# Kernel optimization log

Hardware: AMD Instinct MI355X
Metric: run time of the kernel (lower is better)

The kernel has to match this reference:

```python
import jax, jax.numpy as jnp
import numpy as np

COMPRESSION = 2  # max-pool factor along flattened spatial axis for phi and g


def setup_inputs() -> dict:
    key = jax.random.key(0)
    ks = jax.random.split(key, 5)
    B, C, H, W = 4, 64, 96, 96
    Ci = 32  # intermediate_dim = C // 2
    s = 1.0 / np.sqrt(C)
    return {
        "x": jax.random.normal(ks[0], (B, C, H, W), dtype=jnp.float32),
        "w_theta": jax.random.normal(ks[1], (Ci, C), dtype=jnp.float32) * s,
        "b_theta": jnp.zeros((Ci,), dtype=jnp.float32),
        "w_phi": jax.random.normal(ks[2], (Ci, C), dtype=jnp.float32) * s,
        "b_phi": jnp.zeros((Ci,), dtype=jnp.float32),
        "w_g": jax.random.normal(ks[3], (Ci, C), dtype=jnp.float32) * s,
        "b_g": jnp.zeros((Ci,), dtype=jnp.float32),
        "w_out": jax.random.normal(ks[4], (C, Ci), dtype=jnp.float32) * (1.0 / np.sqrt(Ci)),
        "b_out": jnp.zeros((C,), dtype=jnp.float32),
    }


def reference(x, w_theta, b_theta, w_phi, b_phi, w_g, b_g, w_out, b_out):
    B, C, H, W = x.shape
    N = H * W
    xf = x.reshape(B, C, N).transpose(0, 2, 1)            # [B, N, C]
    # 1x1 conv projections == channel matmuls
    theta = xf @ w_theta.T + b_theta                      # [B, N, Ci]
    phi = xf @ w_phi.T + b_phi                            # [B, N, Ci]
    g = xf @ w_g.T + b_g                                  # [B, N, Ci]
    # compression: max-pool (kernel=stride=COMPRESSION) along flattened spatial axis
    Ci = theta.shape[-1]
    phi = phi.reshape(B, N // COMPRESSION, COMPRESSION, Ci).max(axis=2)  # [B, N/c, Ci]
    g = g.reshape(B, N // COMPRESSION, COMPRESSION, Ci).max(axis=2)      # [B, N/c, Ci]
    # embedded-gaussian affinity + softmax
    attn = jax.nn.softmax(jnp.einsum('bnc,bmc->bnm', theta, phi), axis=-1)  # [B, N, N/c]
    y = jnp.einsum('bnm,bmc->bnc', attn, g)               # [B, N, Ci]
    out = y @ w_out.T + b_out                             # [B, N, C]
    out = out.transpose(0, 2, 1).reshape(B, C, H, W)
    return out + x  # residual
```

## Files before the change

### kernel.cpp

```cpp
#include <hip/hip_runtime.h>
#include <hip/hip_bf16.h>


#define NQ 9216
#define MM 4608
#define LOG2E 1.44269504088896340736f

typedef __attribute__((ext_vector_type(8))) short bf16x8;
typedef __attribute__((ext_vector_type(4))) float f32x4;
typedef __attribute__((ext_vector_type(4))) unsigned short u16x4;

static __device__ __forceinline__ unsigned short f2bf(float f) {
    unsigned u = __float_as_uint(f);
    unsigned r = (u + 0x7fffu + ((u >> 16) & 1u)) >> 16;
    return (unsigned short)r;
}
static __device__ __forceinline__ unsigned pk2(float a, float b) {
    __hip_bfloat162 h = __float22bfloat162_rn(make_float2(a, b));
    return *reinterpret_cast<unsigned*>(&h);
}

__global__ __launch_bounds__(256) void proj_kernel(
    const float* __restrict__ x,
    const float* __restrict__ wt, const float* __restrict__ bt,
    const float* __restrict__ wp, const float* __restrict__ bp,
    const float* __restrict__ wg, const float* __restrict__ bg,
    unsigned short* __restrict__ theta, unsigned short* __restrict__ phi,
    unsigned short* __restrict__ gT, float* __restrict__ pzero)
{
    __shared__ unsigned short gst[32 * 36];

    const int tid  = threadIdx.x;
    const int wid  = tid >> 6;
    const int lane = tid & 63;
    const int q = lane >> 4;
    const int c = lane & 15;

    {
        const int gs = gridDim.x * blockDim.x;
        float4 z4 = {0.f, 0.f, 0.f, 0.f};
        for (int i = blockIdx.x * blockDim.x + tid; i < 304128; i += gs)
            ((float4*)pzero)[i] = z4;
    }

    const int b     = blockIdx.x / 144;
    const int n0blk = (blockIdx.x % 144) * 64;
    const int n0    = n0blk + wid * 16;

    const float* Wm[3] = {wt, wp, wg};
    const float* Bm[3] = {bt, bp, bg};

    bf16x8 wf[3][2][2];
    float bias[3][2];
#pragma unroll
    for (int p = 0; p < 3; ++p) {
#pragma unroll
        for (int ct = 0; ct < 2; ++ct) {
            bias[p][ct] = Bm[p][ct * 16 + c];
#pragma unroll
            for (int ks = 0; ks < 2; ++ks) {
                const float* wsrc = Wm[p] + (ct * 16 + c) * 64 + ks * 32 + q * 8;
                f32x4 w0 = *(const f32x4*)wsrc;
                f32x4 w1 = *(const f32x4*)(wsrc + 4);
                unsigned* wk = (unsigned*)&wf[p][ct][ks];
                wk[0] = pk2(w0[0], w0[1]); wk[1] = pk2(w0[2], w0[3]);
                wk[2] = pk2(w1[0], w1[1]); wk[3] = pk2(w1[2], w1[3]);
            }
        }
    }

    bf16x8 af[2];
#pragma unroll
    for (int ks = 0; ks < 2; ++ks) {
        unsigned* ap = (unsigned*)&af[ks];
#pragma unroll
        for (int j2 = 0; j2 < 4; ++j2) {
            float x0 = x[(b * 64 + ks * 32 + q * 8 + j2 * 2) * NQ + n0 + c];
            float x1 = x[(b * 64 + ks * 32 + q * 8 + j2 * 2 + 1) * NQ + n0 + c];
            ap[j2] = pk2(x0, x1);
        }
    }

#pragma unroll
    for (int p = 0; p < 3; ++p) {
#pragma unroll
        for (int ct = 0; ct < 2; ++ct) {
            f32x4 acc = {0.f, 0.f, 0.f, 0.f};
            acc = __builtin_amdgcn_mfma_f32_16x16x32_bf16(af[0], wf[p][ct][0], acc, 0, 0, 0);
            acc = __builtin_amdgcn_mfma_f32_16x16x32_bf16(af[1], wf[p][ct][1], acc, 0, 0, 0);
#pragma unroll
            for (int r = 0; r < 4; ++r) acc[r] += bias[p][ct];
            const int ci = ct * 16 + c;
            if (p == 0) {
                unsigned pv0 = pk2(acc[0] * LOG2E, acc[1] * LOG2E);
                unsigned pv1 = pk2(acc[2] * LOG2E, acc[3] * LOG2E);
                theta[(b * NQ + n0 + 4 * q + 0) * 32 + ci] = (unsigned short)pv0;
                theta[(b * NQ + n0 + 4 * q + 1) * 32 + ci] = (unsigned short)(pv0 >> 16);
                theta[(b * NQ + n0 + 4 * q + 2) * 32 + ci] = (unsigned short)pv1;
                theta[(b * NQ + n0 + 4 * q + 3) * 32 + ci] = (unsigned short)(pv1 >> 16);
            } else {
                unsigned pv = pk2(fmaxf(acc[0], acc[1]), fmaxf(acc[2], acc[3]));
                if (p == 1) {
                    const int m0 = (n0 >> 1) + 2 * q;
                    phi[(b * MM + m0) * 32 + ci]     = (unsigned short)pv;
                    phi[(b * MM + m0 + 1) * 32 + ci] = (unsigned short)(pv >> 16);
                } else {
                    *(unsigned int*)(gst + ci * 36 + wid * 8 + 2 * q) = pv;
                }
            }
        }
    }

    __syncthreads();
    {
        const int t  = tid & 255;
        const int ci = t >> 3;
        const int m4 = (t & 7) * 4;
        u16x4 v = *(const u16x4*)(gst + ci * 36 + m4);
        *(u16x4*)(gT + (b * 32 + ci) * MM + (n0blk >> 1) + m4) = v;
    }
}

__global__ __launch_bounds__(128, 4) void attn_kernel(
    const unsigned short* __restrict__ theta, const unsigned short* __restrict__ phi,
    const unsigned short* __restrict__ gT,
    float* __restrict__ pacc, float* __restrict__ plsum)
{
    __shared__ unsigned short pld[2][64 * 64];

    const int tid  = threadIdx.x;
    const int w    = tid >> 6;
    const int lane = tid & 63;
    const int q  = lane >> 4;
    const int c  = lane & 15;
    const int xr = (c & 7) << 3;

    const int ks  = blockIdx.x / 288;
    const int rem = blockIdx.x % 288;
    const int b   = rem / 72;
    const int nb  = (rem % 72) * 128 + w * 64;

    bf16x8 qf[4];
#pragma unroll
    for (int rt = 0; rt < 4; ++rt)
        qf[rt] = *(const bf16x8*)(theta + (b * NQ + nb + rt * 16 + c) * 32 + q * 8);

    const unsigned short* phiB = phi + (size_t)b * MM * 32;
    const unsigned short* gTB  = gT + (size_t)b * 32 * MM;
    unsigned short* myp = pld[w];

    f32x4 acc[4][2];
    float lsum[4] = {0.f, 0.f, 0.f, 0.f};
#pragma unroll
    for (int rt = 0; rt < 4; ++rt)
#pragma unroll
        for (int s2 = 0; s2 < 2; ++s2) acc[rt][s2] = (f32x4){0.f, 0.f, 0.f, 0.f};

    const int mt0 = ks * 9;
    bf16x8 kf[4];
#pragma unroll
    for (int mct = 0; mct < 4; ++mct)
        kf[mct] = *(const bf16x8*)(phiB + (mt0 * 64 + mct * 16 + c) * 32 + q * 8);

    for (int mi = 0; mi < 9; ++mi) {
        const int m0  = (mt0 + mi) * 64;
        const int m0n = (mt0 + (mi < 8 ? mi + 1 : mi)) * 64;

        bf16x8 vf[2][2];
#pragma unroll
        for (int s2 = 0; s2 < 2; ++s2)
#pragma unroll
            for (int st = 0; st < 2; ++st)
                vf[s2][st] = *(const bf16x8*)(gTB + (s2 * 16 + c) * MM + m0 + st * 32 + q * 8);

        bf16x8 kn[4];
#pragma unroll
        for (int mct = 0; mct < 4; ++mct)
            kn[mct] = *(const bf16x8*)(phiB + (m0n + mct * 16 + c) * 32 + q * 8);

#pragma unroll
        for (int mct = 0; mct < 4; ++mct) {
#pragma unroll
            for (int rt = 0; rt < 4; ++rt) {
                f32x4 z = {0.f, 0.f, 0.f, 0.f};
                f32x4 s = __builtin_amdgcn_mfma_f32_16x16x32_bf16(kf[mct], qf[rt], z, 0, 0, 0);
                float p0 = __builtin_amdgcn_exp2f(s[0]);
                float p1 = __builtin_amdgcn_exp2f(s[1]);
                float p2 = __builtin_amdgcn_exp2f(s[2]);
                float p3 = __builtin_amdgcn_exp2f(s[3]);
                lsum[rt] += (p0 + p1) + (p2 + p3);
                uint2 hv = {pk2(p0, p1), pk2(p2, p3)};
                *(uint2*)(myp + ((rt * 16 + c) << 6) + ((mct * 16 + 4 * q) ^ xr)) = hv;
            }
        }
#pragma unroll
        for (int rt = 0; rt < 4; ++rt) {
#pragma unroll
            for (int st = 0; st < 2; ++st) {
                bf16x8 pf = *(const bf16x8*)(myp + ((rt * 16 + c) << 6) + ((st * 32 + q * 8) ^ xr));
#pragma unroll
                for (int s2 = 0; s2 < 2; ++s2)
                    acc[rt][s2] = __builtin_amdgcn_mfma_f32_16x16x32_bf16(vf[s2][st], pf, acc[rt][s2], 0, 0, 0);
            }
        }
#pragma unroll
        for (int mct = 0; mct < 4; ++mct) kf[mct] = kn[mct];
    }

#pragma unroll
    for (int rt = 0; rt < 4; ++rt) {
        lsum[rt] += __shfl_xor(lsum[rt], 16);
        lsum[rt] += __shfl_xor(lsum[rt], 32);
    }

#pragma unroll
    for (int rt = 0; rt < 4; ++rt)
#pragma unroll
        for (int s2 = 0; s2 < 2; ++s2)
#pragma unroll
            for (int r = 0; r < 4; ++r)
                atomicAdd(&pacc[(size_t)(b * 32 + s2 * 16 + 4 * q + r) * NQ + nb + rt * 16 + c],
                          acc[rt][s2][r]);
    if (lane < 16) {
#pragma unroll
        for (int rt = 0; rt < 4; ++rt)
            atomicAdd(&plsum[(size_t)b * NQ + nb + rt * 16 + lane], lsum[rt]);
    }
}

__global__ __launch_bounds__(256) void reduce_kernel(
    const float* __restrict__ pacc, const float* __restrict__ plsum,
    const float* __restrict__ w_out, const float* __restrict__ b_out,
    const float* __restrict__ x, float* __restrict__ out)
{
    __shared__ unsigned short yld[32 * 68];

    const int tid = threadIdx.x;
    const int b   = blockIdx.x / 144;
    const int nb  = (blockIdx.x % 144) * 64;

    {
        const int ci = tid >> 3;
        const int n8 = (tid & 7) * 8;
        const float* pr = pacc + (size_t)(b * 32 + ci) * NQ + nb + n8;
        f32x4 a0 = *(const f32x4*)pr;
        f32x4 a1 = *(const f32x4*)(pr + 4);
        const float* lr = plsum + (size_t)b * NQ + nb + n8;
        f32x4 l0 = *(const f32x4*)lr;
        f32x4 l1 = *(const f32x4*)(lr + 4);
        uint2 v0 = {pk2(a0[0] / l0[0], a0[1] / l0[1]), pk2(a0[2] / l0[2], a0[3] / l0[3])};
        uint2 v1 = {pk2(a1[0] / l1[0], a1[1] / l1[1]), pk2(a1[2] / l1[2], a1[3] / l1[3])};
        *(uint2*)(yld + ci * 68 + n8)     = v0;
        *(uint2*)(yld + ci * 68 + n8 + 4) = v1;
    }
    __syncthreads();

    const int w    = tid >> 6;
    const int lane = tid & 63;
    const int q = lane >> 4;
    const int c = lane & 15;

    bf16x8 wof[4];
#pragma unroll
    for (int ct = 0; ct < 4; ++ct) {
        const float* wsrc = w_out + (ct * 16 + c) * 32 + q * 8;
        f32x4 w0 = *(const f32x4*)wsrc;
        f32x4 w1 = *(const f32x4*)(wsrc + 4);
        unsigned* wk = (unsigned*)&wof[ct];
        wk[0] = pk2(w0[0], w0[1]); wk[1] = pk2(w0[2], w0[3]);
        wk[2] = pk2(w1[0], w1[1]); wk[3] = pk2(w1[2], w1[3]);
    }

    bf16x8 yf;
    {
        unsigned short* yp = (unsigned short*)&yf;
#pragma unroll
        for (int j = 0; j < 8; ++j)
            yp[j] = yld[(q * 8 + j) * 68 + w * 16 + c];
    }

#pragma unroll
    for (int ct = 0; ct < 4; ++ct) {
        f32x4 z = {0.f, 0.f, 0.f, 0.f};
        f32x4 o = __builtin_amdgcn_mfma_f32_16x16x32_bf16(wof[ct], yf, z, 0, 0, 0);
#pragma unroll
        for (int r = 0; r < 4; ++r) {
            const int chn = ct * 16 + 4 * q + r;
            const size_t addr = (size_t)(b * 64 + chn) * NQ + nb + w * 16 + c;
            out[addr] = o[r] + b_out[chn] + x[addr];
        }
    }
}

extern "C" void kernel_launch(void* const* d_in, const int* in_sizes, int n_in,
                              void* d_out, int out_size, void* d_ws, size_t ws_size,
                              hipStream_t stream) {
    const float* x       = (const float*)d_in[0];
    const float* w_theta = (const float*)d_in[1];
    const float* b_theta = (const float*)d_in[2];
    const float* w_phi   = (const float*)d_in[3];
    const float* b_phi   = (const float*)d_in[4];
    const float* w_g     = (const float*)d_in[5];
    const float* b_g     = (const float*)d_in[6];
    const float* w_out   = (const float*)d_in[7];
    const float* b_out   = (const float*)d_in[8];
    float* out = (float*)d_out;

    unsigned short* theta = (unsigned short*)d_ws;
    unsigned short* phi   = theta + 4 * NQ * 32;
    unsigned short* gT    = phi + 4 * MM * 32;
    float* pacc  = (float*)(gT + 4 * 32 * MM);
    float* plsum = pacc + (size_t)4 * 32 * NQ;

    proj_kernel<<<576, 256, 0, stream>>>(x, w_theta, b_theta, w_phi, b_phi,
                                         w_g, b_g, theta, phi, gT, pacc);
    attn_kernel<<<8 * 288, 128, 0, stream>>>(theta, phi, gT, pacc, plsum);
    reduce_kernel<<<576, 256, 0, stream>>>(pacc, plsum, w_out, b_out, x, out);
}
```

Baseline: 153.4 us.

## Software-pipeline attention loop, compute row sums via MFMA, halve proj/reduce block size

The attention loop is restructured so that the P·V MFMAs of the previous tile are issued while the next phi/g tiles are loaded and the next exp2 scores are computed. The per-element scalar row-sum adds are replaced by an extra MFMA against a ones vector, which moves that work onto the matrix unit. Occupancy hint changes from 4 to 3 for attn. Projection and reduce kernels now use 128-thread blocks covering 32 positions, giving twice as many blocks.

```diff
diff --git a/kernel.cpp b/kernel.cpp
--- a/kernel.cpp
+++ b/kernel.cpp
@@ -10,17 +10,12 @@
 typedef __attribute__((ext_vector_type(4))) float f32x4;
 typedef __attribute__((ext_vector_type(4))) unsigned short u16x4;
 
-static __device__ __forceinline__ unsigned short f2bf(float f) {
-    unsigned u = __float_as_uint(f);
-    unsigned r = (u + 0x7fffu + ((u >> 16) & 1u)) >> 16;
-    return (unsigned short)r;
-}
 static __device__ __forceinline__ unsigned pk2(float a, float b) {
     __hip_bfloat162 h = __float22bfloat162_rn(make_float2(a, b));
     return *reinterpret_cast<unsigned*>(&h);
 }
 
-__global__ __launch_bounds__(256) void proj_kernel(
+__global__ __launch_bounds__(128, 4) void proj_kernel(
     const float* __restrict__ x,
     const float* __restrict__ wt, const float* __restrict__ bt,
     const float* __restrict__ wp, const float* __restrict__ bp,
@@ -28,7 +23,7 @@
     unsigned short* __restrict__ theta, unsigned short* __restrict__ phi,
     unsigned short* __restrict__ gT, float* __restrict__ pzero)
 {
-    __shared__ unsigned short gst[32 * 36];
+    __shared__ unsigned short gst[32 * 20];
 
     const int tid  = threadIdx.x;
     const int wid  = tid >> 6;
@@ -43,8 +38,9 @@
             ((float4*)pzero)[i] = z4;
     }
 
-    const int b     = blockIdx.x / 144;
-    const int n0blk = (blockIdx.x % 144) * 64;
+    const int b     = blockIdx.x / 288;
+    const int rem   = blockIdx.x % 288;
+    const int n0blk = rem * 32;
     const int n0    = n0blk + wid * 16;
 
     const float* Wm[3] = {wt, wp, wg};
@@ -105,7 +101,7 @@
                     phi[(b * MM + m0) * 32 + ci]     = (unsigned short)pv;
                     phi[(b * MM + m0 + 1) * 32 + ci] = (unsigned short)(pv >> 16);
                 } else {
-                    *(unsigned int*)(gst + ci * 36 + wid * 8 + 2 * q) = pv;
+                    *(unsigned int*)(gst + ci * 20 + wid * 8 + 2 * q) = pv;
                 }
             }
         }
@@ -113,15 +109,14 @@
 
     __syncthreads();
     {
-        const int t  = tid & 255;
-        const int ci = t >> 3;
-        const int m4 = (t & 7) * 4;
-        u16x4 v = *(const u16x4*)(gst + ci * 36 + m4);
-        *(u16x4*)(gT + (b * 32 + ci) * MM + (n0blk >> 1) + m4) = v;
-    }
-}
-
-__global__ __launch_bounds__(128, 4) void attn_kernel(
+        const int ci = tid >> 2;
+        const int m4 = (tid & 3) * 4;
+        u16x4 v = *(const u16x4*)(gst + ci * 20 + m4);
+        *(u16x4*)(gT + (b * 32 + ci) * MM + rem * 16 + m4) = v;
+    }
+}
+
+__global__ __launch_bounds__(128, 3) void attn_kernel(
     const unsigned short* __restrict__ theta, const unsigned short* __restrict__ phi,
     const unsigned short* __restrict__ gT,
     float* __restrict__ pacc, float* __restrict__ plsum)
@@ -145,38 +140,73 @@
     for (int rt = 0; rt < 4; ++rt)
         qf[rt] = *(const bf16x8*)(theta + (b * NQ + nb + rt * 16 + c) * 32 + q * 8);
 
+    bf16x8 onef;
+    {
+        unsigned v = (c == 0) ? 0x3F803F80u : 0u;
+        unsigned* op = (unsigned*)&onef;
+        op[0] = v; op[1] = v; op[2] = v; op[3] = v;
+    }
+
     const unsigned short* phiB = phi + (size_t)b * MM * 32;
     const unsigned short* gTB  = gT + (size_t)b * 32 * MM;
     unsigned short* myp = pld[w];
 
     f32x4 acc[4][2];
-    float lsum[4] = {0.f, 0.f, 0.f, 0.f};
-#pragma unroll
-    for (int rt = 0; rt < 4; ++rt)
+    f32x4 lacc[4];
+#pragma unroll
+    for (int rt = 0; rt < 4; ++rt) {
+        lacc[rt] = (f32x4){0.f, 0.f, 0.f, 0.f};
 #pragma unroll
         for (int s2 = 0; s2 < 2; ++s2) acc[rt][s2] = (f32x4){0.f, 0.f, 0.f, 0.f};
+    }
 
     const int mt0 = ks * 9;
-    bf16x8 kf[4];
+    bf16x8 kf[4], vf[2][2];
+
 #pragma unroll
     for (int mct = 0; mct < 4; ++mct)
         kf[mct] = *(const bf16x8*)(phiB + (mt0 * 64 + mct * 16 + c) * 32 + q * 8);
-
-    for (int mi = 0; mi < 9; ++mi) {
-        const int m0  = (mt0 + mi) * 64;
-        const int m0n = (mt0 + (mi < 8 ? mi + 1 : mi)) * 64;
-
-        bf16x8 vf[2][2];
+#pragma unroll
+    for (int s2 = 0; s2 < 2; ++s2)
+#pragma unroll
+        for (int st = 0; st < 2; ++st)
+            vf[s2][st] = *(const bf16x8*)(gTB + (s2 * 16 + c) * MM + mt0 * 64 + st * 32 + q * 8);
+#pragma unroll
+    for (int mct = 0; mct < 4; ++mct) {
+#pragma unroll
+        for (int rt = 0; rt < 4; ++rt) {
+            f32x4 z = {0.f, 0.f, 0.f, 0.f};
+            f32x4 s = __builtin_amdgcn_mfma_f32_16x16x32_bf16(kf[mct], qf[rt], z, 0, 0, 0);
+            uint2 hv = {pk2(__builtin_amdgcn_exp2f(s[0]), __builtin_amdgcn_exp2f(s[1])),
+                        pk2(__builtin_amdgcn_exp2f(s[2]), __builtin_amdgcn_exp2f(s[3]))};
+            *(uint2*)(myp + ((rt * 16 + c) << 6) + ((mct * 16 + 4 * q) ^ xr)) = hv;
+        }
+    }
+
+    for (int mi = 1; mi < 9; ++mi) {
+        const int m0 = (mt0 + mi) * 64;
+
+#pragma unroll
+        for (int mct = 0; mct < 4; ++mct)
+            kf[mct] = *(const bf16x8*)(phiB + (m0 + mct * 16 + c) * 32 + q * 8);
+
+#pragma unroll
+        for (int rt = 0; rt < 4; ++rt) {
+#pragma unroll
+            for (int st = 0; st < 2; ++st) {
+                bf16x8 pf = *(const bf16x8*)(myp + ((rt * 16 + c) << 6) + ((st * 32 + q * 8) ^ xr));
+#pragma unroll
+                for (int s2 = 0; s2 < 2; ++s2)
+                    acc[rt][s2] = __builtin_amdgcn_mfma_f32_16x16x32_bf16(vf[s2][st], pf, acc[rt][s2], 0, 0, 0);
+                lacc[rt] = __builtin_amdgcn_mfma_f32_16x16x32_bf16(onef, pf, lacc[rt], 0, 0, 0);
+            }
+        }
+
 #pragma unroll
         for (int s2 = 0; s2 < 2; ++s2)
 #pragma unroll
             for (int st = 0; st < 2; ++st)
                 vf[s2][st] = *(const bf16x8*)(gTB + (s2 * 16 + c) * MM + m0 + st * 32 + q * 8);
-
-        bf16x8 kn[4];
-#pragma unroll
-        for (int mct = 0; mct < 4; ++mct)
-            kn[mct] = *(const bf16x8*)(phiB + (m0n + mct * 16 + c) * 32 + q * 8);
 
 #pragma unroll
         for (int mct = 0; mct < 4; ++mct) {
@@ -184,33 +214,23 @@
             for (int rt = 0; rt < 4; ++rt) {
                 f32x4 z = {0.f, 0.f, 0.f, 0.f};
                 f32x4 s = __builtin_amdgcn_mfma_f32_16x16x32_bf16(kf[mct], qf[rt], z, 0, 0, 0);
-                float p0 = __builtin_amdgcn_exp2f(s[0]);
-                float p1 = __builtin_amdgcn_exp2f(s[1]);
-                float p2 = __builtin_amdgcn_exp2f(s[2]);
-                float p3 = __builtin_amdgcn_exp2f(s[3]);
-                lsum[rt] += (p0 + p1) + (p2 + p3);
-                uint2 hv = {pk2(p0, p1), pk2(p2, p3)};
+                uint2 hv = {pk2(__builtin_amdgcn_exp2f(s[0]), __builtin_amdgcn_exp2f(s[1])),
+                            pk2(__builtin_amdgcn_exp2f(s[2]), __builtin_amdgcn_exp2f(s[3]))};
                 *(uint2*)(myp + ((rt * 16 + c) << 6) + ((mct * 16 + 4 * q) ^ xr)) = hv;
             }
         }
-#pragma unroll
-        for (int rt = 0; rt < 4; ++rt) {
-#pragma unroll
-            for (int st = 0; st < 2; ++st) {
-                bf16x8 pf = *(const bf16x8*)(myp + ((rt * 16 + c) << 6) + ((st * 32 + q * 8) ^ xr));
-#pragma unroll
-                for (int s2 = 0; s2 < 2; ++s2)
-                    acc[rt][s2] = __builtin_amdgcn_mfma_f32_16x16x32_bf16(vf[s2][st], pf, acc[rt][s2], 0, 0, 0);
-            }
-        }
-#pragma unroll
-        for (int mct = 0; mct < 4; ++mct) kf[mct] = kn[mct];
     }
 
 #pragma unroll
     for (int rt = 0; rt < 4; ++rt) {
-        lsum[rt] += __shfl_xor(lsum[rt], 16);
-        lsum[rt] += __shfl_xor(lsum[rt], 32);
+#pragma unroll
+        for (int st = 0; st < 2; ++st) {
+            bf16x8 pf = *(const bf16x8*)(myp + ((rt * 16 + c) << 6) + ((st * 32 + q * 8) ^ xr));
+#pragma unroll
+            for (int s2 = 0; s2 < 2; ++s2)
+                acc[rt][s2] = __builtin_amdgcn_mfma_f32_16x16x32_bf16(vf[s2][st], pf, acc[rt][s2], 0, 0, 0);
+            lacc[rt] = __builtin_amdgcn_mfma_f32_16x16x32_bf16(onef, pf, lacc[rt], 0, 0, 0);
+        }
     }
 
 #pragma unroll
@@ -224,24 +244,24 @@
     if (lane < 16) {
 #pragma unroll
         for (int rt = 0; rt < 4; ++rt)
-            atomicAdd(&plsum[(size_t)b * NQ + nb + rt * 16 + lane], lsum[rt]);
-    }
-}
-
-__global__ __launch_bounds__(256) void reduce_kernel(
+            atomicAdd(&plsum[(size_t)b * NQ + nb + rt * 16 + lane], lacc[rt][0]);
+    }
+}
+
+__global__ __launch_bounds__(128, 4) void reduce_kernel(
     const float* __restrict__ pacc, const float* __restrict__ plsum,
     const float* __restrict__ w_out, const float* __restrict__ b_out,
     const float* __restrict__ x, float* __restrict__ out)
 {
-    __shared__ unsigned short yld[32 * 68];
+    __shared__ unsigned short yld[32 * 36];
 
     const int tid = threadIdx.x;
-    const int b   = blockIdx.x / 144;
-    const int nb  = (blockIdx.x % 144) * 64;
-
-    {
-        const int ci = tid >> 3;
-        const int n8 = (tid & 7) * 8;
+    const int b   = blockIdx.x / 288;
+    const int nb  = (blockIdx.x % 288) * 32;
+
+    {
+        const int ci = tid >> 2;
+        const int n8 = (tid & 3) * 8;
         const float* pr = pacc + (size_t)(b * 32 + ci) * NQ + nb + n8;
         f32x4 a0 = *(const f32x4*)pr;
         f32x4 a1 = *(const f32x4*)(pr + 4);
@@ -250,8 +270,8 @@
         f32x4 l1 = *(const f32x4*)(lr + 4);
         uint2 v0 = {pk2(a0[0] / l0[0], a0[1] / l0[1]), pk2(a0[2] / l0[2], a0[3] / l0[3])};
         uint2 v1 = {pk2(a1[0] / l1[0], a1[1] / l1[1]), pk2(a1[2] / l1[2], a1[3] / l1[3])};
-        *(uint2*)(yld + ci * 68 + n8)     = v0;
-        *(uint2*)(yld + ci * 68 + n8 + 4) = v1;
+        *(uint2*)(yld + ci * 36 + n8)     = v0;
+        *(uint2*)(yld + ci * 36 + n8 + 4) = v1;
     }
     __syncthreads();
 
@@ -276,7 +296,7 @@
         unsigned short* yp = (unsigned short*)&yf;
 #pragma unroll
         for (int j = 0; j < 8; ++j)
-            yp[j] = yld[(q * 8 + j) * 68 + w * 16 + c];
+            yp[j] = yld[(q * 8 + j) * 36 + w * 16 + c];
     }
 
 #pragma unroll
@@ -312,8 +332,8 @@
     float* pacc  = (float*)(gT + 4 * 32 * MM);
     float* plsum = pacc + (size_t)4 * 32 * NQ;
 
-    proj_kernel<<<576, 256, 0, stream>>>(x, w_theta, b_theta, w_phi, b_phi,
-                                         w_g, b_g, theta, phi, gT, pacc);
+    proj_kernel<<<1152, 128, 0, stream>>>(x, w_theta, b_theta, w_phi, b_phi,
+                                          w_g, b_g, theta, phi, gT, pacc);
     attn_kernel<<<8 * 288, 128, 0, stream>>>(theta, phi, gT, pacc, plsum);
-    reduce_kernel<<<576, 256, 0, stream>>>(pacc, plsum, w_out, b_out, x, out);
-}
+    reduce_kernel<<<1152, 128, 0, stream>>>(pacc, plsum, w_out, b_out, x, out);
+}
```

Measured after the change: 142.7 us. -7.0%, faster.
